# Optimization experiments

Hardware: AMD Instinct MI355X
Metric: run time of the kernel (lower is better)

Reference implementation:

```python
import jax, jax.numpy as jnp
import numpy as np

N_NODES = 100_000
E_OFF = 1_500_000
LATENT = 64
MP_STEPS = 3


def setup_inputs() -> dict:
    key = jax.random.key(0)
    ks = jax.random.split(key, 12)
    # lower-triangular graph: all self-loops + random off-diagonal edges with row >= col
    r = jax.random.randint(ks[0], (E_OFF,), 0, N_NODES)
    c = jax.random.randint(ks[1], (E_OFF,), 0, N_NODES)
    diag = jnp.arange(N_NODES)
    edge_row = jnp.concatenate([jnp.maximum(r, c), diag]).astype(jnp.int64)
    edge_col = jnp.concatenate([jnp.minimum(r, c), diag]).astype(jnp.int64)
    E = E_OFF + N_NODES
    # positive weights (gcn_norm takes deg^{-1/2} of weighted degree)
    edge_attr = jax.random.uniform(ks[2], (E,), jnp.float32) + 0.05
    x = jax.random.normal(ks[3], (N_NODES, 1), jnp.float32)
    L = LATENT
    def lin(k, fi, fo):
        return jax.random.normal(k, (fi, fo), jnp.float32) / np.sqrt(fi)
    return {
        "x": x,
        "edge_attr": edge_attr,
        "w_enc": lin(ks[4], 1, L), "b_enc": jnp.zeros((L,), jnp.float32),
        "conv1_w": jax.random.normal(ks[5], (MP_STEPS, L, L), jnp.float32) / np.sqrt(L),
        "conv1_b": jnp.zeros((MP_STEPS, L), jnp.float32),
        "conv2_w": jax.random.normal(ks[6], (MP_STEPS, L, L), jnp.float32) / np.sqrt(L),
        "conv2_b": jnp.zeros((MP_STEPS, L), jnp.float32),
        "dec_w1": lin(ks[7], 2 * L, L), "dec_b1": jnp.zeros((L,), jnp.float32),
        "dec_w2": lin(ks[8], L, 1), "dec_b2": jnp.zeros((1,), jnp.float32),
        "edge_row": edge_row,
        "edge_col": edge_col,
    }


def reference(x, edge_attr, w_enc, b_enc, conv1_w, conv1_b, conv2_w, conv2_b,
              dec_w1, dec_b1, dec_w2, dec_b2, edge_row, edge_col):
    N = x.shape[0]
    # GCN normalization (graph already contains all self-loops, so PyG's
    # add_remaining_self_loops is a no-op and keeps existing loop weights)
    deg = jax.ops.segment_sum(edge_attr, edge_col, num_segments=N)
    dinv = jnp.where(deg > 0, jax.lax.rsqrt(jnp.maximum(deg, 1e-30)), 0.0)
    norm = dinv[edge_row] * edge_attr * dinv[edge_col]  # [E]
    cnt = jnp.maximum(
        jax.ops.segment_sum(jnp.ones_like(edge_attr), edge_col, num_segments=N), 1.0
    )[:, None]  # mean aggregation denominator

    def gcn(h, W, b):
        m = (h @ W)[edge_row] * norm[:, None]           # [E, F] messages
        agg = jax.ops.segment_sum(m, edge_col, num_segments=N) / cnt
        return agg + b

    # node encoder: single Linear (no activation)
    h = x @ w_enc + b_enc
    for i in range(MP_STEPS):
        h = jax.nn.relu(gcn(h, conv1_w[i], conv1_b[i]))
        h = jax.nn.relu(gcn(h, conv2_w[i], conv2_b[i]))

    # edge decoder: gather endpoints, MLP [2L -> L -> 1]
    e = jnp.concatenate([h[edge_row], h[edge_col]], axis=1)
    e = jax.nn.relu(e @ dec_w1 + dec_b1)
    e = (e @ dec_w2 + dec_b2)[:, 0]                      # [E]
    vals = jnp.where(edge_row == edge_col, jax.nn.softplus(e), e)
    return vals
```

## Files before the change

### kernel.cpp

```cpp
#include <hip/hip_runtime.h>
#include <hip/hip_fp16.h>
#include <math.h>

#define L 64
#define FIXS 65536.0f
#define WAITCNT_LGKM0 0xC07F

#define FMAMIX_LO(acc, pkh, ws) \
    asm("v_fma_mix_f32 %0, %1, %2, %0 op_sel:[0,0,0] op_sel_hi:[1,0,0]" \
        : "+v"(acc) : "v"(pkh), "v"(ws))
#define FMAMIX_HI(acc, pkh, ws) \
    asm("v_fma_mix_f32 %0, %1, %2, %0 op_sel:[1,0,0] op_sel_hi:[1,0,0]" \
        : "+v"(acc) : "v"(pkh), "v"(ws))
#define PKADDRELU(d, a, b) \
    asm("v_pk_add_f16 %0, %1, %2\n\tv_pk_max_f16 %0, %0, 0" \
        : "=v"(d) : "v"(a), "v"(b))

#define GLOAD(xw_, qv_, J) \
    xw_ = (unsigned)__shfl((int)mwv, (J) * 8 + grp); \
    qv_ = h4[(size_t)(xw_ & 0x1FFFFu) * 8 + sub];
#define FMA8(A, qv_, xw_) { \
    float wv_ = __half2float(__ushort_as_half((unsigned short)((xw_) >> 17))); \
    FMAMIX_LO(A[0], (qv_).x, wv_); FMAMIX_HI(A[1], (qv_).x, wv_); \
    FMAMIX_LO(A[2], (qv_).y, wv_); FMAMIX_HI(A[3], (qv_).y, wv_); \
    FMAMIX_LO(A[4], (qv_).z, wv_); FMAMIX_HI(A[5], (qv_).z, wv_); \
    FMAMIX_LO(A[6], (qv_).w, wv_); FMAMIX_HI(A[7], (qv_).w, wv_); }


__global__ void k_hist(const int* __restrict__ col, const float* __restrict__ attr,
                       unsigned* __restrict__ degcnt,
                       int* __restrict__ rank, int E) {
    int e = blockIdx.x * blockDim.x + threadIdx.x;
    if (e < E) {
        int c = col[e];
        unsigned fx = (unsigned)(int)rintf(attr[e] * FIXS);
        unsigned old = atomicAdd(&degcnt[c], (1u << 24) | fx);
        rank[e] = (int)(old >> 24);
    }
}

__global__ void k_dinv(const unsigned* __restrict__ degcnt,
                       float* __restrict__ dinv, int* __restrict__ cntI,
                       float* __restrict__ rcnt, int N) {
    int n = blockIdx.x * blockDim.x + threadIdx.x;
    if (n < N) {
        unsigned p = degcnt[n];
        unsigned cnt = p >> 24;
        float d = (float)(p & 0xFFFFFFu) * (1.0f / FIXS);
        dinv[n] = (d > 0.f) ? (1.0f / sqrtf(fmaxf(d, 1e-30f))) : 0.f;
        cntI[n] = (int)cnt;
        unsigned c = cnt ? cnt : 1u;
        rcnt[n] = 1.0f / (float)c;
    }
}


__global__ __launch_bounds__(256) void k_scan_a(const int* __restrict__ cntI,
                                                int* __restrict__ blockSums, int N) {
    __shared__ int red[4];
    int b = blockIdx.x, t = threadIdx.x;
    int base = b * 1024 + t * 4;
    int s = 0;
    #pragma unroll
    for (int i = 0; i < 4; ++i) { int idx = base + i; if (idx < N) s += cntI[idx]; }
    #pragma unroll
    for (int off = 32; off > 0; off >>= 1) s += __shfl_down(s, off);
    if ((t & 63) == 0) red[t >> 6] = s;
    __syncthreads();
    if (t == 0) blockSums[b] = red[0] + red[1] + red[2] + red[3];
}

__global__ __launch_bounds__(1024) void k_scan_b(int* __restrict__ blockSums, int B,
                                                 int* __restrict__ ptr, int N) {
    __shared__ int sh[1024];
    int t = threadIdx.x;
    sh[t] = (t < B) ? blockSums[t] : 0;
    __syncthreads();
    for (int off = 1; off < 1024; off <<= 1) {
        int v = (t >= off) ? sh[t - off] : 0;
        __syncthreads();
        sh[t] += v;
        __syncthreads();
    }
    if (t < B) blockSums[t] = (t == 0) ? 0 : sh[t - 1];
    if (t == B - 1) ptr[N] = sh[t];
}

__global__ __launch_bounds__(256) void k_scan_c(const int* __restrict__ cntI,
                                                const int* __restrict__ blockSums,
                                                int* __restrict__ ptr, int N) {
    __shared__ int th[256];
    int b = blockIdx.x, t = threadIdx.x;
    int base = b * 1024 + t * 4;
    int v[4]; int s = 0;
    #pragma unroll
    for (int i = 0; i < 4; ++i) {
        int idx = base + i;
        v[i] = (idx < N) ? cntI[idx] : 0;
        s += v[i];
    }
    th[t] = s;
    __syncthreads();
    for (int off = 1; off < 256; off <<= 1) {
        int xv = (t >= off) ? th[t - off] : 0;
        __syncthreads();
        th[t] += xv;
        __syncthreads();
    }
    int pre = ((t == 0) ? 0 : th[t - 1]) + blockSums[b];
    #pragma unroll
    for (int i = 0; i < 4; ++i) {
        int idx = base + i;
        if (idx < N) ptr[idx] = pre;
        pre += v[i];
    }
}

__global__ void k_scatter(const int* __restrict__ row, const int* __restrict__ col,
                          const float* __restrict__ attr, const float* __restrict__ dinv,
                          const int* __restrict__ colptr,
                          int* __restrict__ rank ,
                          unsigned* __restrict__ csrX, int E) {
    int e = blockIdx.x * blockDim.x + threadIdx.x;
    if (e < E) {
        int r = row[e], c = col[e];
        int pos = colptr[c] + rank[e];
        float nrm = dinv[r] * attr[e] * dinv[c];
        unsigned short nb = __half_as_ushort(__float2half(nrm));
        csrX[pos] = (unsigned)r | ((unsigned)nb << 17);
        rank[e] = pos;
    }
}


__global__ void k_encode(const float* __restrict__ x, const float* __restrict__ w_enc,
                         const float* __restrict__ b_enc, __half* __restrict__ h, int N) {
    int idx = blockIdx.x * blockDim.x + threadIdx.x;
    if (idx < N * L) {
        int n = idx >> 6, f = idx & 63;
        h[idx] = __float2half(x[n] * w_enc[f] + b_enc[f]);
    }
}


__global__ __launch_bounds__(256, 4) void k_gcn(const uint4* __restrict__ h4,
        __half* __restrict__ h_out,
        const float* __restrict__ W, const float* __restrict__ bias,
        const int* __restrict__ colptr, const unsigned* __restrict__ csrX,
        const float* __restrict__ rcnt, int N) {
    __shared__ float sm[4][72];
    int lane = threadIdx.x & 63;
    int warp = threadIdx.x >> 6;
    int grp  = lane >> 3;
    int sub  = lane & 7;
    int wid  = (blockIdx.x * blockDim.x + threadIdx.x) >> 6;
    int nw   = (gridDim.x * blockDim.x) >> 6;
    float* smw = &sm[warp][0];

    float Wc[L];
    #pragma unroll
    for (int f = 0; f < L; ++f) Wc[f] = W[f * L + lane];
    float bl = bias[lane];

    int beg = 0, end = 0; unsigned mw = 0;
    if (wid < N) {
        beg = colptr[wid];
        end = colptr[wid + 1];
        if (beg + lane < end) mw = csrX[beg + lane];
    }

    for (int n = wid; n < N; n += nw) {
        int n2 = n + nw;
        int beg2 = 0, end2 = 0;
        if (n2 < N) { beg2 = colptr[n2]; end2 = colptr[n2 + 1]; }
        float rcv = rcnt[n];

        float va[8], vb[8];
        #pragma unroll
        for (int i = 0; i < 8; ++i) { va[i] = 0.f; vb[i] = 0.f; }

        auto PROC = [&](unsigned mwv, int mm) {
            int kmax = (mm + 7) >> 3;
            int k = 0;
            while (k < kmax) {
                int rem = kmax - k;
                if (rem >= 4) {
                    unsigned x0, x1, x2, x3; uint4 q0, q1, q2, q3;
                    GLOAD(x0, q0, k) GLOAD(x1, q1, k + 1)
                    GLOAD(x2, q2, k + 2) GLOAD(x3, q3, k + 3)
                    FMA8(va, q0, x0) FMA8(vb, q1, x1)
                    FMA8(va, q2, x2) FMA8(vb, q3, x3)
                    k += 4;
                } else if (rem == 3) {
                    unsigned x0, x1, x2; uint4 q0, q1, q2;
                    GLOAD(x0, q0, k) GLOAD(x1, q1, k + 1) GLOAD(x2, q2, k + 2)
                    FMA8(va, q0, x0) FMA8(vb, q1, x1) FMA8(va, q2, x2)
                    k += 3;
                } else if (rem == 2) {
                    unsigned x0, x1; uint4 q0, q1;
                    GLOAD(x0, q0, k) GLOAD(x1, q1, k + 1)
                    FMA8(va, q0, x0) FMA8(vb, q1, x1)
                    k += 2;
                } else {
                    unsigned x0; uint4 q0;
                    GLOAD(x0, q0, k)
                    FMA8(va, q0, x0)
                    k += 1;
                }
            }
        };

        int m = end - beg; if (m > 64) m = 64;
        PROC(mw, m);
        for (int base = beg + 64; base < end; base += 64) {
            int mm = end - base; if (mm > 64) mm = 64;
            unsigned mwc = 0;
            if (lane < mm) mwc = csrX[base + lane];
            PROC(mwc, mm);
        }

        unsigned mw2 = 0;
        if (n2 < N && beg2 + lane < end2) mw2 = csrX[beg2 + lane];

        float s[8];
        #pragma unroll
        for (int i = 0; i < 8; ++i) {
            float v = va[i] + vb[i];
            v += __shfl_xor(v, 8);
            v += __shfl_xor(v, 16);
            v += __shfl_xor(v, 32);
            s[i] = v;
        }
        if (lane < 8) {
            #pragma unroll
            for (int i = 0; i < 8; ++i) smw[8 * lane + i] = s[i];
        }
        __builtin_amdgcn_s_waitcnt(WAITCNT_LGKM0);
        float a0 = 0.f, a1 = 0.f, a2 = 0.f, a3 = 0.f;
        const float4* smv = (const float4*)smw;
        #pragma unroll
        for (int q = 0; q < 16; ++q) {
            float4 sv = smv[q];
            a0 += sv.x * Wc[4 * q + 0];
            a1 += sv.y * Wc[4 * q + 1];
            a2 += sv.z * Wc[4 * q + 2];
            a3 += sv.w * Wc[4 * q + 3];
        }
        float o = ((a0 + a1) + (a2 + a3)) * rcv + bl;
        h_out[(size_t)n * L + lane] = __float2half(fmaxf(o, 0.f));

        beg = beg2; end = end2; mw = mw2;
    }
}


__global__ __launch_bounds__(256, 2) void k_mv2(const __half* __restrict__ h,
        const float* __restrict__ W1, const float* __restrict__ b1,
        __half* __restrict__ U, __half* __restrict__ V, int N) {
    __shared__ float sm[4][72];
    int lane = threadIdx.x & 63;
    int warp = threadIdx.x >> 6;
    int wid  = (blockIdx.x * blockDim.x + threadIdx.x) >> 6;
    int nw   = (gridDim.x * blockDim.x) >> 6;
    float* smw = &sm[warp][0];
    float Wu[L], Wv[L];
    #pragma unroll
    for (int f = 0; f < L; ++f) Wu[f] = W1[f * L + lane];
    #pragma unroll
    for (int f = 0; f < L; ++f) Wv[f] = W1[(L + f) * L + lane];
    float bl = b1[lane];
    for (int n = wid; n < N; n += nw) {
        float hl = __half2float(h[(size_t)n * L + lane]);
        smw[lane] = hl;
        __builtin_amdgcn_s_waitcnt(WAITCNT_LGKM0);
        float a0 = 0.f, a1 = 0.f, c0 = 0.f, c1 = 0.f;
        const float4* smv = (const float4*)smw;
        #pragma unroll
        for (int q = 0; q < 16; ++q) {
            float4 sv = smv[q];
            a0 += sv.x * Wu[4 * q + 0] ; a1 += sv.y * Wu[4 * q + 1];
            a0 += sv.z * Wu[4 * q + 2] ; a1 += sv.w * Wu[4 * q + 3];
            c0 += sv.x * Wv[4 * q + 0] ; c1 += sv.y * Wv[4 * q + 1];
            c0 += sv.z * Wv[4 * q + 2] ; c1 += sv.w * Wv[4 * q + 3];
        }
        U[(size_t)n * L + lane] = __float2half((a0 + a1) + bl);
        V[(size_t)n * L + lane] = __float2half(c0 + c1);
        __builtin_amdgcn_s_waitcnt(WAITCNT_LGKM0);
    }
}


__global__ __launch_bounds__(256) void k_edge(const __half* __restrict__ U,
        const __half* __restrict__ V, const float* __restrict__ w2,
        const float* __restrict__ b2,
        const int* __restrict__ colptr, const unsigned* __restrict__ csrX,
        float* __restrict__ tmp, int N) {
    int lane = threadIdx.x & 63;
    int hf   = lane & 1;
    int wid  = (blockIdx.x * blockDim.x + threadIdx.x) >> 6;
    int nw   = (gridDim.x * blockDim.x) >> 6;
    float w2f[32];
    #pragma unroll
    for (int k = 0; k < 32; ++k) w2f[k] = w2[32 * hf + k];
    float b2v = b2[0];

    int beg = 0, end = 0; unsigned md0 = 0;
    if (wid < N) {
        beg = colptr[wid]; end = colptr[wid + 1];
        int ep = beg + (lane >> 1);
        if (ep < end) md0 = csrX[ep];
    }

    for (int n = wid; n < N; n += nw) {
        int n2 = n + nw;
        int beg2 = 0, end2 = 0;
        if (n2 < N) { beg2 = colptr[n2]; end2 = colptr[n2 + 1]; }

        const uint4* vrow = (const uint4*)(V + (size_t)n * L + 32 * hf);
        uint4 v0 = vrow[0], v1 = vrow[1], v2 = vrow[2], v3 = vrow[3];
        unsigned md = md0;
        for (int base = beg; base < end; base += 32) {
            int epos = base + (lane >> 1);
            if (epos < end) {
                int r = (int)(md & 0x1FFFFu);
                const uint4* urow = (const uint4*)(U + (size_t)r * L + 32 * hf);
                uint4 u0 = urow[0], u1 = urow[1], u2 = urow[2], u3 = urow[3];
                float p0 = 0.f, p1 = 0.f, p2 = 0.f, p3 = 0.f;
                #define DOT2X(uw_, vw_, B, pa, pb) { unsigned t_; \
                    PKADDRELU(t_, (uw_), (vw_)); \
                    FMAMIX_LO(pa, t_, w2f[B]); FMAMIX_HI(pb, t_, w2f[(B) + 1]); }
                DOT2X(u0.x, v0.x,  0, p0, p1) DOT2X(u0.y, v0.y,  2, p2, p3)
                DOT2X(u0.z, v0.z,  4, p0, p1) DOT2X(u0.w, v0.w,  6, p2, p3)
                DOT2X(u1.x, v1.x,  8, p0, p1) DOT2X(u1.y, v1.y, 10, p2, p3)
                DOT2X(u1.z, v1.z, 12, p0, p1) DOT2X(u1.w, v1.w, 14, p2, p3)
                DOT2X(u2.x, v2.x, 16, p0, p1) DOT2X(u2.y, v2.y, 18, p2, p3)
                DOT2X(u2.z, v2.z, 20, p0, p1) DOT2X(u2.w, v2.w, 22, p2, p3)
                DOT2X(u3.x, v3.x, 24, p0, p1) DOT2X(u3.y, v3.y, 26, p2, p3)
                DOT2X(u3.z, v3.z, 28, p0, p1) DOT2X(u3.w, v3.w, 30, p2, p3)
                #undef DOT2X
                float p = (p0 + p2) + (p1 + p3);
                p += __shfl_xor(p, 1);
                if (hf == 0) {
                    float val = p + b2v;
                    if (r == n) val = fmaxf(val, 0.f) + log1pf(expf(-fabsf(val)));
                    tmp[epos] = val;
                }
            }
            if (base + 32 < end) {
                int ep2 = base + 32 + (lane >> 1);
                md = (ep2 < end) ? csrX[ep2] : 0;
            }
        }

        unsigned mdn = 0;
        if (n2 < N) {
            int ep = beg2 + (lane >> 1);
            if (ep < end2) mdn = csrX[ep];
        }
        beg = beg2; end = end2; md0 = mdn;
    }
}


__global__ void k_perm(const int* __restrict__ epos, const float* __restrict__ tmp,
                       float* __restrict__ out, int E) {
    int e = blockIdx.x * blockDim.x + threadIdx.x;
    if (e < E) out[e] = tmp[epos[e]];
}


extern "C" void kernel_launch(void* const* d_in, const int* in_sizes, int n_in,
                              void* d_out, int out_size, void* d_ws, size_t ws_size,
                              hipStream_t stream) {
    const float* x     = (const float*)d_in[0];
    const float* attr  = (const float*)d_in[1];
    const float* w_enc = (const float*)d_in[2];
    const float* b_enc = (const float*)d_in[3];
    const float* c1w   = (const float*)d_in[4];
    const float* c1b   = (const float*)d_in[5];
    const float* c2w   = (const float*)d_in[6];
    const float* c2b   = (const float*)d_in[7];
    const float* dw1   = (const float*)d_in[8];
    const float* db1   = (const float*)d_in[9];
    const float* dw2   = (const float*)d_in[10];
    const float* db2   = (const float*)d_in[11];
    const int*   erow  = (const int*)d_in[12];
    const int*   ecol  = (const int*)d_in[13];
    int N = in_sizes[0];
    int E = in_sizes[1];
    float* out = (float*)d_out;

    char* w = (char*)d_ws;
    auto alloc = [&](size_t bytes) {
        char* p = w; w += (bytes + 255) & ~(size_t)255; return p;
    };
    unsigned* degcnt = (unsigned*)alloc((size_t)N * 4);
    size_t zbytes = (size_t)(w - (char*)d_ws);
    float* dinv   = (float*)alloc((size_t)N * 4);
    int*   cntI   = (int*)  alloc((size_t)N * 4);
    float* rcnt   = (float*)alloc((size_t)N * 4);
    int*   colptr = (int*)  alloc((size_t)(N + 1) * 4);
    int*   bsums  = (int*)  alloc(((size_t)(N + 1023) / 1024 + 1) * 4);
    int*   rank   = (int*)  alloc((size_t)E * 4);
    unsigned* csrX = (unsigned*)alloc((size_t)E * 4);
    float* tmp    = (float*)alloc((size_t)E * 4);
    __half* hA    = (__half*)alloc((size_t)N * L * 2);
    __half* hB    = (__half*)alloc((size_t)N * L * 2);
    __half* hU    = (__half*)alloc((size_t)N * L * 2);
    __half* hV    = (__half*)alloc((size_t)N * L * 2);
    (void)ws_size; (void)n_in; (void)out_size;

    (void)hipMemsetAsync(d_ws, 0, zbytes, stream);

    int eb = (E + 255) / 256;
    int nb = (N + 255) / 256;
    int B  = (N + 1023) / 1024;
    k_hist<<<eb, 256, 0, stream>>>(ecol, attr, degcnt, rank, E);
    k_dinv<<<nb, 256, 0, stream>>>(degcnt, dinv, cntI, rcnt, N);
    k_scan_a<<<B, 256, 0, stream>>>(cntI, bsums, N);
    k_scan_b<<<1, 1024, 0, stream>>>(bsums, B, colptr, N);
    k_scan_c<<<B, 256, 0, stream>>>(cntI, bsums, colptr, N);
    k_scatter<<<eb, 256, 0, stream>>>(erow, ecol, attr, dinv, colptr, rank, csrX, E);
    k_encode<<<(N * L + 255) / 256, 256, 0, stream>>>(x, w_enc, b_enc, hA, N);

    __half* hin = hA; __half* hout = hB;
    for (int i = 0; i < 3; ++i) {
        k_gcn<<<2048, 256, 0, stream>>>((const uint4*)hin, hout, c1w + i * L * L,
                                        c1b + i * L, colptr, csrX, rcnt, N);
        __half* t = hin; hin = hout; hout = t;
        k_gcn<<<2048, 256, 0, stream>>>((const uint4*)hin, hout, c2w + i * L * L,
                                        c2b + i * L, colptr, csrX, rcnt, N);
        t = hin; hin = hout; hout = t;
    }
    k_mv2<<<2048, 256, 0, stream>>>(hin, dw1, db1, hU, hV, N);
    k_edge<<<2048, 256, 0, stream>>>(hU, hV, dw2, db2, colptr, csrX, tmp, N);
    k_perm<<<eb, 256, 0, stream>>>(rank, tmp, out, E);
}
```

Before: 648.1 us.

## Split GCN into transform-then-aggregate and fold encoder into first conv weight

Each GCN layer is restructured from aggregate-then-multiply into a separate dense transform kernel (k_gx computing h@W) followed by a sparse aggregation kernel (k_agg) with bias, mean and ReLU. The aggregation kernel no longer holds 64 weight registers, which allows higher occupancy (launch bounds 6) and lets it write 8 halfs per lane with vectorized stores. The encoder Linear is folded into the first conv weight on the device, so the first layer starts directly from x*we1+be1. The cost is five extra kernel launches, an extra read and write of the N×64 feature matrix per layer, and extra fp16 rounding of the transformed features before they are aggregated.

```diff
diff --git a/kernel.cpp b/kernel.cpp
--- a/kernel.cpp
+++ b/kernel.cpp
@@ -119,7 +119,7 @@
 __global__ void k_scatter(const int* __restrict__ row, const int* __restrict__ col,
                           const float* __restrict__ attr, const float* __restrict__ dinv,
                           const int* __restrict__ colptr,
-                          int* __restrict__ rank ,
+                          int* __restrict__ rank,
                           unsigned* __restrict__ csrX, int E) {
     int e = blockIdx.x * blockDim.x + threadIdx.x;
     if (e < E) {
@@ -133,34 +133,75 @@
 }
 
 
-__global__ void k_encode(const float* __restrict__ x, const float* __restrict__ w_enc,
-                         const float* __restrict__ b_enc, __half* __restrict__ h, int N) {
+__global__ void k_fold(const float* __restrict__ w_enc, const float* __restrict__ b_enc,
+                       const float* __restrict__ W1,
+                       float* __restrict__ we1, float* __restrict__ be1) {
+    int j = threadIdx.x;
+    if (j < L) {
+        float a = 0.f, b = 0.f;
+        for (int f = 0; f < L; ++f) {
+            float wv = W1[f * L + j];
+            a += w_enc[f] * wv;
+            b += b_enc[f] * wv;
+        }
+        we1[j] = a; be1[j] = b;
+    }
+}
+
+__global__ void k_encode(const float* __restrict__ x, const float* __restrict__ we1,
+                         const float* __restrict__ be1, __half* __restrict__ g, int N) {
     int idx = blockIdx.x * blockDim.x + threadIdx.x;
     if (idx < N * L) {
         int n = idx >> 6, f = idx & 63;
-        h[idx] = __float2half(x[n] * w_enc[f] + b_enc[f]);
-    }
-}
-
-
-__global__ __launch_bounds__(256, 4) void k_gcn(const uint4* __restrict__ h4,
-        __half* __restrict__ h_out,
-        const float* __restrict__ W, const float* __restrict__ bias,
-        const int* __restrict__ colptr, const unsigned* __restrict__ csrX,
-        const float* __restrict__ rcnt, int N) {
+        g[idx] = __float2half(x[n] * we1[f] + be1[f]);
+    }
+}
+
+
+__global__ __launch_bounds__(256, 4) void k_gx(const __half* __restrict__ h,
+        const float* __restrict__ W, __half* __restrict__ g, int N) {
     __shared__ float sm[4][72];
     int lane = threadIdx.x & 63;
     int warp = threadIdx.x >> 6;
+    int wid  = (blockIdx.x * blockDim.x + threadIdx.x) >> 6;
+    int nw   = (gridDim.x * blockDim.x) >> 6;
+    float* smw = &sm[warp][0];
+    float Wc[L];
+    #pragma unroll
+    for (int f = 0; f < L; ++f) Wc[f] = W[f * L + lane];
+    for (int n = wid; n < N; n += nw) {
+        float hl = __half2float(h[(size_t)n * L + lane]);
+        smw[lane] = hl;
+        __builtin_amdgcn_s_waitcnt(WAITCNT_LGKM0);
+        float a0 = 0.f, a1 = 0.f, a2 = 0.f, a3 = 0.f;
+        const float4* smv = (const float4*)smw;
+        #pragma unroll
+        for (int q = 0; q < 16; ++q) {
+            float4 sv = smv[q];
+            a0 += sv.x * Wc[4 * q + 0];
+            a1 += sv.y * Wc[4 * q + 1];
+            a2 += sv.z * Wc[4 * q + 2];
+            a3 += sv.w * Wc[4 * q + 3];
+        }
+        g[(size_t)n * L + lane] = __float2half((a0 + a1) + (a2 + a3));
+        __builtin_amdgcn_s_waitcnt(WAITCNT_LGKM0);
+    }
+}
+
+
+__global__ __launch_bounds__(256, 6) void k_agg(const uint4* __restrict__ h4,
+        __half* __restrict__ h_out, const float* __restrict__ bias,
+        const int* __restrict__ colptr, const unsigned* __restrict__ csrX,
+        const float* __restrict__ rcnt, int N) {
+    int lane = threadIdx.x & 63;
     int grp  = lane >> 3;
     int sub  = lane & 7;
     int wid  = (blockIdx.x * blockDim.x + threadIdx.x) >> 6;
     int nw   = (gridDim.x * blockDim.x) >> 6;
-    float* smw = &sm[warp][0];
-
-    float Wc[L];
-    #pragma unroll
-    for (int f = 0; f < L; ++f) Wc[f] = W[f * L + lane];
-    float bl = bias[lane];
+
+    float bl8[8];
+    #pragma unroll
+    for (int i = 0; i < 8; ++i) bl8[i] = bias[8 * sub + i];
 
     int beg = 0, end = 0; unsigned mw = 0;
     if (wid < N) {
@@ -232,22 +273,17 @@
             s[i] = v;
         }
         if (lane < 8) {
+            unsigned u[4];
             #pragma unroll
-            for (int i = 0; i < 8; ++i) smw[8 * lane + i] = s[i];
-        }
-        __builtin_amdgcn_s_waitcnt(WAITCNT_LGKM0);
-        float a0 = 0.f, a1 = 0.f, a2 = 0.f, a3 = 0.f;
-        const float4* smv = (const float4*)smw;
-        #pragma unroll
-        for (int q = 0; q < 16; ++q) {
-            float4 sv = smv[q];
-            a0 += sv.x * Wc[4 * q + 0];
-            a1 += sv.y * Wc[4 * q + 1];
-            a2 += sv.z * Wc[4 * q + 2];
-            a3 += sv.w * Wc[4 * q + 3];
-        }
-        float o = ((a0 + a1) + (a2 + a3)) * rcv + bl;
-        h_out[(size_t)n * L + lane] = __float2half(fmaxf(o, 0.f));
+            for (int i = 0; i < 4; ++i) {
+                float oa = fmaxf(s[2 * i]     * rcv + bl8[2 * i],     0.f);
+                float ob = fmaxf(s[2 * i + 1] * rcv + bl8[2 * i + 1], 0.f);
+                u[i] = (unsigned)__half_as_ushort(__float2half(oa))
+                     | ((unsigned)__half_as_ushort(__float2half(ob)) << 16);
+            }
+            uint4 st; st.x = u[0]; st.y = u[1]; st.z = u[2]; st.w = u[3];
+            ((uint4*)h_out)[(size_t)n * 8 + lane] = st;
+        }
 
         beg = beg2; end = end2; mw = mw2;
     }
@@ -401,6 +437,8 @@
     float* rcnt   = (float*)alloc((size_t)N * 4);
     int*   colptr = (int*)  alloc((size_t)(N + 1) * 4);
     int*   bsums  = (int*)  alloc(((size_t)(N + 1023) / 1024 + 1) * 4);
+    float* we1    = (float*)alloc(L * 4);
+    float* be1    = (float*)alloc(L * 4);
     int*   rank   = (int*)  alloc((size_t)E * 4);
     unsigned* csrX = (unsigned*)alloc((size_t)E * 4);
     float* tmp    = (float*)alloc((size_t)E * 4);
@@ -408,6 +446,7 @@
     __half* hB    = (__half*)alloc((size_t)N * L * 2);
     __half* hU    = (__half*)alloc((size_t)N * L * 2);
     __half* hV    = (__half*)alloc((size_t)N * L * 2);
+    __half* gbuf  = hU;
     (void)ws_size; (void)n_in; (void)out_size;
 
     (void)hipMemsetAsync(d_ws, 0, zbytes, stream);
@@ -421,18 +460,27 @@
     k_scan_b<<<1, 1024, 0, stream>>>(bsums, B, colptr, N);
     k_scan_c<<<B, 256, 0, stream>>>(cntI, bsums, colptr, N);
     k_scatter<<<eb, 256, 0, stream>>>(erow, ecol, attr, dinv, colptr, rank, csrX, E);
-    k_encode<<<(N * L + 255) / 256, 256, 0, stream>>>(x, w_enc, b_enc, hA, N);
-
-    __half* hin = hA; __half* hout = hB;
-    for (int i = 0; i < 3; ++i) {
-        k_gcn<<<2048, 256, 0, stream>>>((const uint4*)hin, hout, c1w + i * L * L,
-                                        c1b + i * L, colptr, csrX, rcnt, N);
-        __half* t = hin; hin = hout; hout = t;
-        k_gcn<<<2048, 256, 0, stream>>>((const uint4*)hin, hout, c2w + i * L * L,
-                                        c2b + i * L, colptr, csrX, rcnt, N);
-        t = hin; hin = hout; hout = t;
-    }
-    k_mv2<<<2048, 256, 0, stream>>>(hin, dw1, db1, hU, hV, N);
+
+    k_fold<<<1, 64, 0, stream>>>(w_enc, b_enc, c1w, we1, be1);
+    k_encode<<<(N * L + 255) / 256, 256, 0, stream>>>(x, we1, be1, gbuf, N);
+
+    const float* Ws[6] = {c1w,            c2w,
+                          c1w + L * L,    c2w + L * L,
+                          c1w + 2 * L * L, c2w + 2 * L * L};
+    const float* Bs[6] = {c1b,         c2b,
+                          c1b + L,     c2b + L,
+                          c1b + 2 * L, c2b + 2 * L};
+    (void)Ws[0];
+    __half* outs[2] = {hA, hB};
+    __half* hcur = nullptr;
+    for (int j = 0; j < 6; ++j) {
+        hcur = outs[j & 1];
+        k_agg<<<2048, 256, 0, stream>>>((const uint4*)gbuf, hcur, Bs[j],
+                                        colptr, csrX, rcnt, N);
+        if (j < 5)
+            k_gx<<<2048, 256, 0, stream>>>(hcur, Ws[j + 1], gbuf, N);
+    }
+    k_mv2<<<2048, 256, 0, stream>>>(hcur, dw1, db1, hU, hV, N);
     k_edge<<<2048, 256, 0, stream>>>(hU, hV, dw2, db2, colptr, csrX, tmp, N);
     k_perm<<<eb, 256, 0, stream>>>(rank, tmp, out, E);
 }
```

Result: slower. 696.5 us (+7.5%).

## Parallelize edge decoder over flat edges with 8 lanes per edge

Applied to the files above, without the earlier changes.

Changes the edge decoder from one wavefront per destination node (two lanes per edge, V row held in registers) to a flat loop over CSR edge positions, with 8 lanes per edge each handling 8 features. A per-edge destination-column array is written during scatter so the edge kernel no longer needs colptr. The softplus for self-loops moves into the permutation kernel, which now reads erow and ecol. The aim is to remove load imbalance and idle lanes on low-degree nodes. The cost is an extra array write and read, a V row gather on every edge, and two more index reads in k_perm.

```diff
diff --git a/kernel.cpp b/kernel.cpp
--- a/kernel.cpp
+++ b/kernel.cpp
@@ -119,8 +119,8 @@
 __global__ void k_scatter(const int* __restrict__ row, const int* __restrict__ col,
                           const float* __restrict__ attr, const float* __restrict__ dinv,
                           const int* __restrict__ colptr,
-                          int* __restrict__ rank ,
-                          unsigned* __restrict__ csrX, int E) {
+                          int* __restrict__ rank,
+                          unsigned* __restrict__ csrX, int* __restrict__ colof, int E) {
     int e = blockIdx.x * blockDim.x + threadIdx.x;
     if (e < E) {
         int r = row[e], c = col[e];
@@ -128,6 +128,7 @@
         float nrm = dinv[r] * attr[e] * dinv[c];
         unsigned short nb = __half_as_ushort(__float2half(nrm));
         csrX[pos] = (unsigned)r | ((unsigned)nb << 17);
+        colof[pos] = c;
         rank[e] = pos;
     }
 }
@@ -290,82 +291,49 @@
 }
 
 
-__global__ __launch_bounds__(256) void k_edge(const __half* __restrict__ U,
+__global__ __launch_bounds__(256, 8) void k_edge(const __half* __restrict__ U,
         const __half* __restrict__ V, const float* __restrict__ w2,
-        const float* __restrict__ b2,
-        const int* __restrict__ colptr, const unsigned* __restrict__ csrX,
-        float* __restrict__ tmp, int N) {
-    int lane = threadIdx.x & 63;
-    int hf   = lane & 1;
-    int wid  = (blockIdx.x * blockDim.x + threadIdx.x) >> 6;
-    int nw   = (gridDim.x * blockDim.x) >> 6;
-    float w2f[32];
-    #pragma unroll
-    for (int k = 0; k < 32; ++k) w2f[k] = w2[32 * hf + k];
+        const float* __restrict__ b2, const unsigned* __restrict__ csrX,
+        const int* __restrict__ colof, float* __restrict__ tmp, int E) {
+    int sub = threadIdx.x & 7;
+    float w2f[8];
+    #pragma unroll
+    for (int i = 0; i < 8; ++i) w2f[i] = w2[8 * sub + i];
     float b2v = b2[0];
-
-    int beg = 0, end = 0; unsigned md0 = 0;
-    if (wid < N) {
-        beg = colptr[wid]; end = colptr[wid + 1];
-        int ep = beg + (lane >> 1);
-        if (ep < end) md0 = csrX[ep];
-    }
-
-    for (int n = wid; n < N; n += nw) {
-        int n2 = n + nw;
-        int beg2 = 0, end2 = 0;
-        if (n2 < N) { beg2 = colptr[n2]; end2 = colptr[n2 + 1]; }
-
-        const uint4* vrow = (const uint4*)(V + (size_t)n * L + 32 * hf);
-        uint4 v0 = vrow[0], v1 = vrow[1], v2 = vrow[2], v3 = vrow[3];
-        unsigned md = md0;
-        for (int base = beg; base < end; base += 32) {
-            int epos = base + (lane >> 1);
-            if (epos < end) {
-                int r = (int)(md & 0x1FFFFu);
-                const uint4* urow = (const uint4*)(U + (size_t)r * L + 32 * hf);
-                uint4 u0 = urow[0], u1 = urow[1], u2 = urow[2], u3 = urow[3];
-                float p0 = 0.f, p1 = 0.f, p2 = 0.f, p3 = 0.f;
-                #define DOT2X(uw_, vw_, B, pa, pb) { unsigned t_; \
-                    PKADDRELU(t_, (uw_), (vw_)); \
-                    FMAMIX_LO(pa, t_, w2f[B]); FMAMIX_HI(pb, t_, w2f[(B) + 1]); }
-                DOT2X(u0.x, v0.x,  0, p0, p1) DOT2X(u0.y, v0.y,  2, p2, p3)
-                DOT2X(u0.z, v0.z,  4, p0, p1) DOT2X(u0.w, v0.w,  6, p2, p3)
-                DOT2X(u1.x, v1.x,  8, p0, p1) DOT2X(u1.y, v1.y, 10, p2, p3)
-                DOT2X(u1.z, v1.z, 12, p0, p1) DOT2X(u1.w, v1.w, 14, p2, p3)
-                DOT2X(u2.x, v2.x, 16, p0, p1) DOT2X(u2.y, v2.y, 18, p2, p3)
-                DOT2X(u2.z, v2.z, 20, p0, p1) DOT2X(u2.w, v2.w, 22, p2, p3)
-                DOT2X(u3.x, v3.x, 24, p0, p1) DOT2X(u3.y, v3.y, 26, p2, p3)
-                DOT2X(u3.z, v3.z, 28, p0, p1) DOT2X(u3.w, v3.w, 30, p2, p3)
-                #undef DOT2X
-                float p = (p0 + p2) + (p1 + p3);
-                p += __shfl_xor(p, 1);
-                if (hf == 0) {
-                    float val = p + b2v;
-                    if (r == n) val = fmaxf(val, 0.f) + log1pf(expf(-fabsf(val)));
-                    tmp[epos] = val;
-                }
-            }
-            if (base + 32 < end) {
-                int ep2 = base + 32 + (lane >> 1);
-                md = (ep2 < end) ? csrX[ep2] : 0;
-            }
-        }
-
-        unsigned mdn = 0;
-        if (n2 < N) {
-            int ep = beg2 + (lane >> 1);
-            if (ep < end2) mdn = csrX[ep];
-        }
-        beg = beg2; end = end2; md0 = mdn;
+    int tid = blockIdx.x * blockDim.x + threadIdx.x;
+    int np  = (gridDim.x * blockDim.x) >> 3;
+    for (int p = tid >> 3; p < E; p += np) {
+        unsigned md = csrX[p];
+        int r = (int)(md & 0x1FFFFu);
+        int n = colof[p];
+        uint4 uq = ((const uint4*)(U + (size_t)r * L))[sub];
+        uint4 vq = ((const uint4*)(V + (size_t)n * L))[sub];
+        float p0 = 0.f, p1 = 0.f;
+        #define DOT2X(uw_, vw_, B) { unsigned t_; \
+            PKADDRELU(t_, (uw_), (vw_)); \
+            FMAMIX_LO(p0, t_, w2f[B]); FMAMIX_HI(p1, t_, w2f[(B) + 1]); }
+        DOT2X(uq.x, vq.x, 0) DOT2X(uq.y, vq.y, 2)
+        DOT2X(uq.z, vq.z, 4) DOT2X(uq.w, vq.w, 6)
+        #undef DOT2X
+        float pd = p0 + p1;
+        pd += __shfl_xor(pd, 1);
+        pd += __shfl_xor(pd, 2);
+        pd += __shfl_xor(pd, 4);
+        if (sub == 0) tmp[p] = pd + b2v;
     }
 }
 
 
 __global__ void k_perm(const int* __restrict__ epos, const float* __restrict__ tmp,
+                       const int* __restrict__ erow, const int* __restrict__ ecol,
                        float* __restrict__ out, int E) {
     int e = blockIdx.x * blockDim.x + threadIdx.x;
-    if (e < E) out[e] = tmp[epos[e]];
+    if (e < E) {
+        float val = tmp[epos[e]];
+        if (erow[e] == ecol[e])
+            val = fmaxf(val, 0.f) + log1pf(expf(-fabsf(val)));
+        out[e] = val;
+    }
 }
 
 
@@ -403,6 +371,7 @@
     int*   bsums  = (int*)  alloc(((size_t)(N + 1023) / 1024 + 1) * 4);
     int*   rank   = (int*)  alloc((size_t)E * 4);
     unsigned* csrX = (unsigned*)alloc((size_t)E * 4);
+    int*   colof  = (int*)  alloc((size_t)E * 4);
     float* tmp    = (float*)alloc((size_t)E * 4);
     __half* hA    = (__half*)alloc((size_t)N * L * 2);
     __half* hB    = (__half*)alloc((size_t)N * L * 2);
@@ -420,7 +389,8 @@
     k_scan_a<<<B, 256, 0, stream>>>(cntI, bsums, N);
     k_scan_b<<<1, 1024, 0, stream>>>(bsums, B, colptr, N);
     k_scan_c<<<B, 256, 0, stream>>>(cntI, bsums, colptr, N);
-    k_scatter<<<eb, 256, 0, stream>>>(erow, ecol, attr, dinv, colptr, rank, csrX, E);
+    k_scatter<<<eb, 256, 0, stream>>>(erow, ecol, attr, dinv, colptr, rank,
+                                      csrX, colof, E);
     k_encode<<<(N * L + 255) / 256, 256, 0, stream>>>(x, w_enc, b_enc, hA, N);
 
     __half* hin = hA; __half* hout = hB;
@@ -433,6 +403,6 @@
         t = hin; hin = hout; hout = t;
     }
     k_mv2<<<2048, 256, 0, stream>>>(hin, dw1, db1, hU, hV, N);
-    k_edge<<<2048, 256, 0, stream>>>(hU, hV, dw2, db2, colptr, csrX, tmp, N);
-    k_perm<<<eb, 256, 0, stream>>>(rank, tmp, out, E);
-}
+    k_edge<<<2048, 256, 0, stream>>>(hU, hV, dw2, db2, csrX, colof, tmp, E);
+    k_perm<<<eb, 256, 0, stream>>>(rank, tmp, erow, ecol, out, E);
+}
```

Measured after the change: 634.8 us. -2.1%, faster.
